# Optimization experiments

Hardware: AMD Instinct MI355X
Metric: run time of the kernel (lower is better)

## Reference

```python
import jax, jax.numpy as jnp
import numpy as np

B, T, F, U = 256, 512, 64, 128
MAX_TIMESTAMP = 100.0


def setup_inputs() -> dict:
    key = jax.random.key(0)
    ks = jax.random.split(key, 16)

    def w(k, shape, scale=0.05):
        return jax.random.normal(k, shape, dtype=jnp.float32) * scale

    return {
        "inputs": jax.random.uniform(ks[0], (B, T, 5 * F), dtype=jnp.float32),
        "h0": jnp.zeros((B, U), jnp.float32),
        "ts0": jnp.zeros((B, F), jnp.float32),
        "dt0": jnp.zeros((B, F), jnp.float32),
        "w_regression": w(ks[1], (U, F)),
        "b_regression": jnp.zeros((1,), jnp.float32),
        "w_controleur": w(ks[2], (U, F)),
        "b_controleur": jnp.zeros((F,), jnp.float32),
        "w_delta": w(ks[3], (F, U)),
        "b_delta": jnp.zeros((1,), jnp.float32),
        "w_value_mask": w(ks[4], (2 * F, U)),
        "b_value_mask": jnp.zeros((1,), jnp.float32),
        "w_corr": w(ks[5], (F, F)),
        "b_corr": jnp.zeros((F,), jnp.float32),
        "w_concat": w(ks[6], (F + U, F)),
        "b_concat": jnp.zeros((1,), jnp.float32),
        "u_update": w(ks[7], (U, U)),
        "w_update": w(ks[8], (2 * F, U)),
        "b_update": jnp.zeros((1,), jnp.float32),
        "u_reset": w(ks[9], (U, U)),
        "w_reset": w(ks[10], (2 * F, U)),
        "b_reset": jnp.zeros((1,), jnp.float32),
    }


def reference(inputs, h0, ts0, dt0,
              w_regression, b_regression, w_controleur, b_controleur,
              w_delta, b_delta, w_value_mask, b_value_mask,
              w_corr, b_corr, w_concat, b_concat,
              u_update, w_update, b_update,
              u_reset, w_reset, b_reset):
    nf = ts0.shape[1]
    off_diag = (1.0 - jnp.eye(nf, dtype=inputs.dtype))  # zero-diagonal mask on w_corr
    w_corr_masked = off_diag * w_corr

    def step(carry, x_t):
        h, prev_ts, prev_dt = carry
        ti = x_t[:, :nf]
        x_cur = x_t[:, nf:2 * nf]
        m = x_t[:, 2 * nf:3 * nf]
        dt = x_t[:, 3 * nf:4 * nf]
        pad = x_t[:, 4 * nf:5 * nf]

        x_reg = h @ w_regression + b_regression          # [B,F]
        # timestamp generation branch (is_timestamps_generated=True)
        tv = jnp.abs(h @ w_controleur + b_controleur)    # [B,F]
        ti = pad * ti + (1.0 - pad) * (prev_ts + tv)
        ti = jnp.where(ti <= MAX_TIMESTAMP, ti, prev_ts)
        d_gen = jnp.where(prev_ts + tv <= MAX_TIMESTAMP, tv, prev_dt)
        dt = pad * dt + (1.0 - pad) * d_gen

        x_cur = m * x_cur + (1.0 - m) * x_reg
        decay = jnp.exp(-jax.nn.relu(dt @ w_delta + b_delta))   # [B,U]
        z_corr = x_cur @ w_corr_masked + b_corr                  # [B,F]
        beta = jax.nn.sigmoid(jnp.concatenate([m, decay], 1) @ w_concat + b_concat)
        c_t = beta * z_corr + (1.0 - beta) * x_reg
        c = m * x_cur + (1.0 - m) * c_t

        cm = jnp.concatenate([c, m], 1)                  # [B,2F]
        dh = decay * h                                   # [B,U]
        z = jax.nn.sigmoid(dh @ u_update + cm @ w_update + b_update)
        r = jax.nn.sigmoid(dh @ u_reset + cm @ w_reset + b_reset)
        # NOTE: original code (faithfully) uses u_update in the candidate
        h_hat = jnp.tanh((r * dh) @ u_update + cm @ w_value_mask + b_value_mask)
        h_new = (1.0 - z) * h + z * h_hat

        out = jnp.concatenate([x_reg, z_corr, c, ti, dt], 1)  # [B,5F]
        return (h_new, ti, dt), out

    xs = jnp.swapaxes(inputs, 0, 1)  # [T,B,5F]
    (hT, tsT, dtT), out_seq = jax.lax.scan(step, (h0, ts0, dt0), xs)
    return out_seq, hT, tsT, dtT
```

## Files before the change

### kernel.cpp

```cpp
#include <hip/hip_runtime.h>
#include <stdint.h>


#define T_STEPS 512
#define BDIM 512

typedef unsigned int u32;
typedef u32 u32x4 __attribute__((ext_vector_type(4)));
typedef __fp16 f16;
typedef f16 h2 __attribute__((ext_vector_type(2)));

union pun { u32 u; h2 h; };
__device__ __forceinline__ u32 h2u(h2 h) { pun p; p.h = h; return p.u; }
__device__ __forceinline__ h2 u2h(u32 u) { pun p; p.u = u; return p.h; }
__device__ __forceinline__ h2 pkh(float a, float b) { return __builtin_amdgcn_cvt_pkrtz(a, b); }

__device__ __forceinline__ float dot2(h2 a, h2 b, float c) {
    return __builtin_amdgcn_fdot2(a, b, c, false);
}
__device__ __forceinline__ float sigm(float x) { return 1.0f / (1.0f + __expf(-x)); }
__device__ __forceinline__ float tanh_f(float x) { return 2.0f / (1.0f + __expf(-2.0f * x)) - 1.0f; }

__global__ __launch_bounds__(BDIM) __attribute__((amdgpu_waves_per_eu(2, 2)))
void padd_gru_kernel(
    const float* __restrict__ xin,
    const float* __restrict__ h0,
    const float* __restrict__ ts0,
    const float* __restrict__ dt0,
    const float* __restrict__ w_reg, const float* __restrict__ b_reg,
    const float* __restrict__ w_ctl, const float* __restrict__ b_ctl,
    const float* __restrict__ w_dlt, const float* __restrict__ b_dlt,
    const float* __restrict__ w_vm,  const float* __restrict__ b_vm,
    const float* __restrict__ w_cor, const float* __restrict__ b_cor,
    const float* __restrict__ w_cat, const float* __restrict__ b_cat,
    const float* __restrict__ u_upd, const float* __restrict__ w_upd, const float* __restrict__ b_upd,
    const float* __restrict__ u_rst, const float* __restrict__ w_rst, const float* __restrict__ b_rst,
    float* __restrict__ out)
{
    const int t = threadIdx.x;
    const int b = blockIdx.x;

    __shared__ float h32[128];
    __shared__ float outbuf[320];
    __shared__ float tv32[64];
    __shared__ float xcur32[64];
    __shared__ float m32[64];
    __shared__ float dh32[128];
    __shared__ float z32[128];
    __shared__ float xs[320];
    __shared__ float bctl32[64];
    __shared__ float bcor32[64];
    __shared__ __align__(16) u32 hpk[64];
    __shared__ __align__(16) u32 dtpk[32];
    __shared__ __align__(16) u32 xcpk[32];
    __shared__ __align__(16) u32 catpk[96];
    __shared__ __align__(16) u32 epk[128];
    __shared__ __align__(16) u32 rdhpk[64];

    const int s4 = t & 3, j4 = t >> 2;
    const int s8 = t & 7, j8 = t >> 3;
    const int s2 = t & 1, j2 = t >> 1;

    h2 wA[16];
    h2 wD[8];
    h2 wC[4];
    h2 wCt[12];
    h2 wE[64];
    h2 wF[32];

    {
        const float* src = (j4 < 64) ? (w_reg + j4) : (w_ctl + (j4 - 64));
        #pragma unroll
        for (int i = 0; i < 16; i++) {
            int k = 32 * s4 + 2 * i;
            wA[i] = pkh(src[k * 64], src[(k + 1) * 64]);
        }
    }
    {
        #pragma unroll
        for (int i = 0; i < 8; i++) {
            int k = 16 * s4 + 2 * i;
            wD[i] = pkh(w_dlt[k * 128 + j4], w_dlt[(k + 1) * 128 + j4]);
        }
    }
    {
        #pragma unroll
        for (int i = 0; i < 4; i++) {
            int k = 8 * s8 + 2 * i;
            float a = (k     == j8) ? 0.f : w_cor[k * 64 + j8];
            float c = (k + 1 == j8) ? 0.f : w_cor[(k + 1) * 64 + j8];
            wC[i] = pkh(a, c);
        }
    }
    {
        #pragma unroll
        for (int i = 0; i < 12; i++) {
            int k = 24 * s8 + 2 * i;
            wCt[i] = pkh(w_cat[k * 64 + j8], w_cat[(k + 1) * 64 + j8]);
        }
    }
    {
        const float* M = (j2 < 128) ? (s2 == 0 ? u_upd : w_upd)
                                    : (s2 == 0 ? u_rst : w_rst);
        const float* src = M + (j2 & 127);
        #pragma unroll
        for (int i = 0; i < 64; i++) {
            wE[i] = pkh(src[(2 * i) * 128], src[(2 * i + 1) * 128]);
        }
    }
    {
        const float* base = (s4 < 2) ? (u_upd + (64 * s4) * 128 + j4)
                                     : (w_vm + (64 * (s4 - 2)) * 128 + j4);
        #pragma unroll
        for (int i = 0; i < 32; i++) {
            wF[i] = pkh(base[(2 * i) * 128], base[(2 * i + 1) * 128]);
        }
    }

    const float bReg = b_reg[0];
    const float bDlt = b_dlt[0];
    const float bVm  = b_vm[0];
    const float bCat = b_cat[0];
    const float bUpd = b_upd[0];
    const float bRst = b_rst[0];

    if (t < 128) h32[t] = h0[(size_t)b * 128 + t];
    if (t < 64) {
        outbuf[192 + t] = ts0[(size_t)b * 64 + t];
        outbuf[256 + t] = dt0[(size_t)b * 64 + t];
        bctl32[t] = b_ctl[t];
        bcor32[t] = b_cor[t];
        hpk[t] = h2u(pkh(h0[(size_t)b * 128 + 2 * t], h0[(size_t)b * 128 + 2 * t + 1]));
    }

    float2 xpre;
    xpre.x = 0.f; xpre.y = 0.f;
    if (t < 160) {
        xpre = ((const float2*)(xin + (size_t)b * 512 * 320))[t];
    }

    __syncthreads();

    for (int st = 0; st < T_STEPS; ++st) {
        if (t < 160) {
            xs[2 * t]     = xpre.x;
            xs[2 * t + 1] = xpre.y;
            int stn = (st + 1 < T_STEPS) ? (st + 1) : st;
            xpre = ((const float2*)(xin + ((size_t)b * 512 + stn) * 320))[t];
        }

        {
            const u32x4* hp = (const u32x4*)&hpk[16 * s4];
            float a0 = 0.f, a1 = 0.f;
            #pragma unroll
            for (int q = 0; q < 4; q++) {
                u32x4 h4 = hp[q];
                a0 = dot2(wA[4*q+0], u2h(h4.x), a0);
                a1 = dot2(wA[4*q+1], u2h(h4.y), a1);
                a0 = dot2(wA[4*q+2], u2h(h4.z), a0);
                a1 = dot2(wA[4*q+3], u2h(h4.w), a1);
            }
            float v = a0 + a1;
            v += __shfl_xor(v, 1);
            v += __shfl_xor(v, 2);
            if (s4 == 0) {
                if (j4 < 64) outbuf[j4] = v + bReg;
                else         tv32[j4 - 64] = fabsf(v + bctl32[j4 - 64]);
            }
        }
        __syncthreads();

        if (t < 64) {
            float ti_in = xs[t], x_in = xs[64 + t], m = xs[128 + t];
            float dt_in = xs[192 + t], pad = xs[256 + t];
            float pts = outbuf[192 + t], pdt = outbuf[256 + t];
            float tv = tv32[t], xrg = outbuf[t];
            float sum = pts + tv;
            float tic = pad * ti_in + (1.f - pad) * sum;
            float tin = (tic <= 100.0f) ? tic : pts;
            float dg  = (sum <= 100.0f) ? tv : pdt;
            float dtn = pad * dt_in + (1.f - pad) * dg;
            float xc  = m * x_in + (1.f - m) * xrg;
            outbuf[192 + t] = tin;
            outbuf[256 + t] = dtn;
            xcur32[t] = xc;
            m32[t] = m;
            float dtn2 = __shfl_down(dtn, 1);
            float xc2  = __shfl_down(xc, 1);
            float m2   = __shfl_down(m, 1);
            if ((t & 1) == 0) {
                dtpk[t >> 1] = h2u(pkh(dtn, dtn2));
                xcpk[t >> 1] = h2u(pkh(xc, xc2));
                u32 mp = h2u(pkh(m, m2));
                catpk[t >> 1] = mp;
                epk[96 + (t >> 1)] = mp;
            }
        }
        __syncthreads();

        {
            const u32x4* dp = (const u32x4*)&dtpk[8 * s4];
            float a0 = 0.f, a1 = 0.f;
            #pragma unroll
            for (int q = 0; q < 2; q++) {
                u32x4 d4 = dp[q];
                a0 = dot2(wD[4*q+0], u2h(d4.x), a0);
                a1 = dot2(wD[4*q+1], u2h(d4.y), a1);
                a0 = dot2(wD[4*q+2], u2h(d4.z), a0);
                a1 = dot2(wD[4*q+3], u2h(d4.w), a1);
            }
            float vd = a0 + a1;
            vd += __shfl_xor(vd, 1);
            vd += __shfl_xor(vd, 2);

            u32x4 x4 = *(const u32x4*)&xcpk[4 * s8];
            float c0 = dot2(wC[0], u2h(x4.x), 0.f);
            float c1 = dot2(wC[1], u2h(x4.y), 0.f);
            c0 = dot2(wC[2], u2h(x4.z), c0);
            c1 = dot2(wC[3], u2h(x4.w), c1);
            float vc = c0 + c1;
            vc += __shfl_xor(vc, 1);
            vc += __shfl_xor(vc, 2);
            vc += __shfl_xor(vc, 4);

            float d  = __expf(-fmaxf(vd + bDlt, 0.f));
            float dh = d * h32[j4];
            float d2  = __shfl_down(d, 4);
            float dh2 = __shfl_down(dh, 4);
            if (s4 == 0) dh32[j4] = dh;
            if ((t & 7) == 0) {
                catpk[32 + (j4 >> 1)] = h2u(pkh(d, d2));
                epk[j4 >> 1]          = h2u(pkh(dh, dh2));
                outbuf[64 + j8] = vc + bcor32[j8];
            }
        }
        __syncthreads();

        {
            const u32x4* cp = (const u32x4*)&catpk[12 * s8];
            float a0 = 0.f, a1 = 0.f;
            #pragma unroll
            for (int q = 0; q < 3; q++) {
                u32x4 c4 = cp[q];
                a0 = dot2(wCt[4*q+0], u2h(c4.x), a0);
                a1 = dot2(wCt[4*q+1], u2h(c4.y), a1);
                a0 = dot2(wCt[4*q+2], u2h(c4.z), a0);
                a1 = dot2(wCt[4*q+3], u2h(c4.w), a1);
            }
            float v = a0 + a1;
            v += __shfl_xor(v, 1);
            v += __shfl_xor(v, 2);
            v += __shfl_xor(v, 4);
            float beta = sigm(v + bCat);
            float ct = beta * outbuf[64 + j8] + (1.f - beta) * outbuf[j8];
            float m  = m32[j8];
            float c  = m * xcur32[j8] + (1.f - m) * ct;
            float c2 = __shfl_down(c, 8);
            if (s8 == 0) outbuf[128 + j8] = c;
            if ((t & 15) == 0) epk[64 + (j8 >> 1)] = h2u(pkh(c, c2));
        }
        __syncthreads();

        {
            const u32x4* ep = (const u32x4*)&epk[64 * s2];
            float a0 = 0.f, a1 = 0.f, a2 = 0.f, a3 = 0.f;
            #pragma unroll
            for (int q = 0; q < 16; q++) {
                u32x4 e4 = ep[q];
                a0 = dot2(wE[4*q+0], u2h(e4.x), a0);
                a1 = dot2(wE[4*q+1], u2h(e4.y), a1);
                a2 = dot2(wE[4*q+2], u2h(e4.z), a2);
                a3 = dot2(wE[4*q+3], u2h(e4.w), a3);
            }
            float v = (a0 + a1) + (a2 + a3);
            v += __shfl_xor(v, 1);
            if (j2 < 128) {
                float z = sigm(v + bUpd);
                if (s2 == 0) z32[j2] = z;
            } else {
                float r = sigm(v + bRst);
                float rdh = r * dh32[j2 - 128];
                float rdh2 = __shfl_down(rdh, 2);
                if ((t & 3) == 0) rdhpk[(j2 - 128) >> 1] = h2u(pkh(rdh, rdh2));
            }
            if (t < 160) {
                float2 v2;
                v2.x = outbuf[2 * t];
                v2.y = outbuf[2 * t + 1];
                ((float2*)(out + ((size_t)st * 256 + b) * 320))[t] = v2;
            }
        }
        __syncthreads();

        {
            const u32x4* fp = (s4 & 2) ? (const u32x4*)&epk[64 + 32 * (s4 & 1)]
                                       : (const u32x4*)&rdhpk[32 * s4];
            float a0 = 0.f, a1 = 0.f;
            #pragma unroll
            for (int q = 0; q < 8; q++) {
                u32x4 f4 = fp[q];
                a0 = dot2(wF[4*q+0], u2h(f4.x), a0);
                a1 = dot2(wF[4*q+1], u2h(f4.y), a1);
                a0 = dot2(wF[4*q+2], u2h(f4.z), a0);
                a1 = dot2(wF[4*q+3], u2h(f4.w), a1);
            }
            float v = a0 + a1;
            v += __shfl_xor(v, 1);
            v += __shfl_xor(v, 2);
            float hh = tanh_f(v + bVm);
            float z = z32[j4];
            float hn = (1.f - z) * h32[j4] + z * hh;
            float hn2 = __shfl_down(hn, 4);
            if (s4 == 0) h32[j4] = hn;
            if ((t & 7) == 0) hpk[j4 >> 1] = h2u(pkh(hn, hn2));
        }
        __syncthreads();
    }

    if (t < 128) out[(size_t)41943040u + (size_t)b * 128 + t] = h32[t];
    if (t < 64) {
        out[(size_t)41975808u + (size_t)b * 64 + t] = outbuf[192 + t];
        out[(size_t)41992192u + (size_t)b * 64 + t] = outbuf[256 + t];
    }
}

extern "C" void kernel_launch(void* const* d_in, const int* in_sizes, int n_in,
                              void* d_out, int out_size, void* d_ws, size_t ws_size,
                              hipStream_t stream) {
    const float* xin   = (const float*)d_in[0];
    const float* h0    = (const float*)d_in[1];
    const float* ts0   = (const float*)d_in[2];
    const float* dt0   = (const float*)d_in[3];
    const float* w_reg = (const float*)d_in[4];
    const float* b_reg = (const float*)d_in[5];
    const float* w_ctl = (const float*)d_in[6];
    const float* b_ctl = (const float*)d_in[7];
    const float* w_dlt = (const float*)d_in[8];
    const float* b_dlt = (const float*)d_in[9];
    const float* w_vm  = (const float*)d_in[10];
    const float* b_vm  = (const float*)d_in[11];
    const float* w_cor = (const float*)d_in[12];
    const float* b_cor = (const float*)d_in[13];
    const float* w_cat = (const float*)d_in[14];
    const float* b_cat = (const float*)d_in[15];
    const float* u_upd = (const float*)d_in[16];
    const float* w_upd = (const float*)d_in[17];
    const float* b_upd = (const float*)d_in[18];
    const float* u_rst = (const float*)d_in[19];
    const float* w_rst = (const float*)d_in[20];
    const float* b_rst = (const float*)d_in[21];

    padd_gru_kernel<<<dim3(256), dim3(BDIM), 0, stream>>>(
        xin, h0, ts0, dt0,
        w_reg, b_reg, w_ctl, b_ctl, w_dlt, b_dlt, w_vm, b_vm,
        w_cor, b_cor, w_cat, b_cat,
        u_upd, w_upd, b_upd, u_rst, w_rst, b_rst,
        (float*)d_out);
}
```

Before: 1.496 ms.

## Remap lanes for DPP/permlane reductions and fold elementwise stage into matvec

Result: faster. 1.340 ms (-10.4%).

```diff
diff --git a/kernel.cpp b/kernel.cpp
--- a/kernel.cpp
+++ b/kernel.cpp
@@ -21,7 +21,43 @@
 __device__ __forceinline__ float sigm(float x) { return 1.0f / (1.0f + __expf(-x)); }
 __device__ __forceinline__ float tanh_f(float x) { return 2.0f / (1.0f + __expf(-2.0f * x)) - 1.0f; }
 
-__global__ __launch_bounds__(BDIM) __attribute__((amdgpu_waves_per_eu(2, 2)))
+template<int CTRL>
+__device__ __forceinline__ float qadd(float v) {
+    int p = __builtin_amdgcn_update_dpp(0, __float_as_int(v), CTRL, 0xF, 0xF, true);
+    return v + __int_as_float(p);
+}
+template<int CTRL>
+__device__ __forceinline__ float qxchg(float v) {
+    return __int_as_float(__builtin_amdgcn_update_dpp(0, __float_as_int(v), CTRL, 0xF, 0xF, true));
+}
+__device__ __forceinline__ float x16sum(float v) {
+#if __has_builtin(__builtin_amdgcn_permlane16_swap)
+    auto r = __builtin_amdgcn_permlane16_swap(__float_as_uint(v), __float_as_uint(v), false, false);
+    return __uint_as_float(r[0]) + __uint_as_float(r[1]);
+#else
+    return v + __shfl_xor(v, 16);
+#endif
+}
+__device__ __forceinline__ float x16get(float v, int l) {
+#if __has_builtin(__builtin_amdgcn_permlane16_swap)
+    auto r = __builtin_amdgcn_permlane16_swap(__float_as_uint(v), __float_as_uint(v), false, false);
+    return __uint_as_float((l & 16) ? r[0] : r[1]);
+#else
+    return __shfl_xor(v, 16);
+#endif
+}
+__device__ __forceinline__ float x32get(float v, int l) {
+#if __has_builtin(__builtin_amdgcn_permlane32_swap)
+    auto r = __builtin_amdgcn_permlane32_swap(__float_as_uint(v), __float_as_uint(v), false, false);
+    return __uint_as_float((l & 32) ? r[0] : r[1]);
+#else
+    return __shfl_xor(v, 32);
+#endif
+}
+
+__device__ __forceinline__ int klo(int p) { return (p & 3) + 8 * (p >> 2); }
+
+__global__ __launch_bounds__(BDIM, 2)
 void padd_gru_kernel(
     const float* __restrict__ xin,
     const float* __restrict__ h0,
@@ -42,7 +78,6 @@
 
     __shared__ float h32[128];
     __shared__ float outbuf[320];
-    __shared__ float tv32[64];
     __shared__ float xcur32[64];
     __shared__ float m32[64];
     __shared__ float dh32[128];
@@ -57,9 +92,15 @@
     __shared__ __align__(16) u32 epk[128];
     __shared__ __align__(16) u32 rdhpk[64];
 
-    const int s4 = t & 3, j4 = t >> 2;
-    const int s8 = t & 7, j8 = t >> 3;
-    const int s2 = t & 1, j2 = t >> 1;
+    const int l = t & 63, w = t >> 6;
+    const int sA = l & 3;
+    const int b23 = (l >> 2) & 3;
+    const int b4 = (l >> 4) & 1, b5 = (l >> 5) & 1;
+    const int fA = b23 + 4 * b5 + 8 * w;
+    const int uCF = b23 + 4 * ((l >> 4) & 3) + 16 * w;
+    const int s8 = (l & 3) | (b4 << 2);
+    const int s2 = l & 1;
+    const int jE = ((l >> 1) & 31) + 32 * w;
 
     h2 wA[16];
     h2 wD[8];
@@ -69,51 +110,61 @@
     h2 wF[32];
 
     {
-        const float* src = (j4 < 64) ? (w_reg + j4) : (w_ctl + (j4 - 64));
+        const float* src = b4 ? (w_ctl + fA) : (w_reg + fA);
         #pragma unroll
         for (int i = 0; i < 16; i++) {
-            int k = 32 * s4 + 2 * i;
-            wA[i] = pkh(src[k * 64], src[(k + 1) * 64]);
+            int k = klo(16 * sA + i);
+            wA[i] = pkh(src[k * 64], src[(k + 4) * 64]);
         }
     }
     {
         #pragma unroll
         for (int i = 0; i < 8; i++) {
-            int k = 16 * s4 + 2 * i;
-            wD[i] = pkh(w_dlt[k * 128 + j4], w_dlt[(k + 1) * 128 + j4]);
+            int k = klo(8 * sA + i);
+            wD[i] = pkh(w_dlt[k * 128 + uCF], w_dlt[(k + 4) * 128 + uCF]);
         }
     }
     {
         #pragma unroll
         for (int i = 0; i < 4; i++) {
-            int k = 8 * s8 + 2 * i;
-            float a = (k     == j8) ? 0.f : w_cor[k * 64 + j8];
-            float c = (k + 1 == j8) ? 0.f : w_cor[(k + 1) * 64 + j8];
+            int k = klo(4 * s8 + i);
+            float a = (k     == fA) ? 0.f : w_cor[k * 64 + fA];
+            float c = (k + 4 == fA) ? 0.f : w_cor[(k + 4) * 64 + fA];
             wC[i] = pkh(a, c);
         }
     }
     {
         #pragma unroll
         for (int i = 0; i < 12; i++) {
-            int k = 24 * s8 + 2 * i;
-            wCt[i] = pkh(w_cat[k * 64 + j8], w_cat[(k + 1) * 64 + j8]);
-        }
-    }
-    {
-        const float* M = (j2 < 128) ? (s2 == 0 ? u_upd : w_upd)
-                                    : (s2 == 0 ? u_rst : w_rst);
-        const float* src = M + (j2 & 127);
+            int sig = 12 * s8 + i;
+            int r0 = (sig < 32) ? klo(sig) : 64 + klo(sig - 32);
+            wCt[i] = pkh(w_cat[r0 * 64 + fA], w_cat[(r0 + 4) * 64 + fA]);
+        }
+    }
+    {
+        const float* MU = (jE < 128) ? u_upd : u_rst;
+        const float* MW = (jE < 128) ? w_upd : w_rst;
+        const int cj = jE & 127;
         #pragma unroll
         for (int i = 0; i < 64; i++) {
-            wE[i] = pkh(src[(2 * i) * 128], src[(2 * i + 1) * 128]);
-        }
-    }
-    {
-        const float* base = (s4 < 2) ? (u_upd + (64 * s4) * 128 + j4)
-                                     : (w_vm + (64 * (s4 - 2)) * 128 + j4);
+            int sig = 64 * s2 + i;
+            const float* M; int r0;
+            if (sig < 64)      { M = MU; r0 = klo(sig); }
+            else if (sig < 96) { M = MW; r0 = klo(sig - 64); }
+            else               { M = MW; r0 = 64 + klo(sig - 96); }
+            wE[i] = pkh(M[r0 * 128 + cj], M[(r0 + 4) * 128 + cj]);
+        }
+    }
+    {
         #pragma unroll
         for (int i = 0; i < 32; i++) {
-            wF[i] = pkh(base[(2 * i) * 128], base[(2 * i + 1) * 128]);
+            int sig = 32 * sA + i;
+            if (sig < 64) {
+                wF[i] = pkh(u_upd[(2 * sig) * 128 + uCF], u_upd[(2 * sig + 1) * 128 + uCF]);
+            } else {
+                int k = (sig < 96) ? klo(sig - 64) : 64 + klo(sig - 96);
+                wF[i] = pkh(w_vm[k * 128 + uCF], w_vm[(k + 4) * 128 + uCF]);
+            }
         }
     }
 
@@ -130,27 +181,21 @@
         outbuf[256 + t] = dt0[(size_t)b * 64 + t];
         bctl32[t] = b_ctl[t];
         bcor32[t] = b_cor[t];
-        hpk[t] = h2u(pkh(h0[(size_t)b * 128 + 2 * t], h0[(size_t)b * 128 + 2 * t + 1]));
-    }
-
-    float2 xpre;
-    xpre.x = 0.f; xpre.y = 0.f;
+        int u = klo(t);
+        hpk[t] = h2u(pkh(h0[(size_t)b * 128 + u], h0[(size_t)b * 128 + u + 4]));
+    }
+
+    float2 xpre; xpre.x = 0.f; xpre.y = 0.f;
     if (t < 160) {
-        xpre = ((const float2*)(xin + (size_t)b * 512 * 320))[t];
-    }
-
+        float2 x0 = ((const float2*)(xin + (size_t)b * 512 * 320))[t];
+        xs[2 * t] = x0.x; xs[2 * t + 1] = x0.y;
+        xpre = ((const float2*)(xin + ((size_t)b * 512 + 1) * 320))[t];
+    }
     __syncthreads();
 
     for (int st = 0; st < T_STEPS; ++st) {
-        if (t < 160) {
-            xs[2 * t]     = xpre.x;
-            xs[2 * t + 1] = xpre.y;
-            int stn = (st + 1 < T_STEPS) ? (st + 1) : st;
-            xpre = ((const float2*)(xin + ((size_t)b * 512 + stn) * 320))[t];
-        }
-
-        {
-            const u32x4* hp = (const u32x4*)&hpk[16 * s4];
+        {
+            const u32x4* hp = (const u32x4*)&hpk[16 * sA];
             float a0 = 0.f, a1 = 0.f;
             #pragma unroll
             for (int q = 0; q < 4; q++) {
@@ -160,46 +205,39 @@
                 a0 = dot2(wA[4*q+2], u2h(h4.z), a0);
                 a1 = dot2(wA[4*q+3], u2h(h4.w), a1);
             }
-            float v = a0 + a1;
-            v += __shfl_xor(v, 1);
-            v += __shfl_xor(v, 2);
-            if (s4 == 0) {
-                if (j4 < 64) outbuf[j4] = v + bReg;
-                else         tv32[j4 - 64] = fabsf(v + bctl32[j4 - 64]);
-            }
-        }
-        __syncthreads();
-
-        if (t < 64) {
-            float ti_in = xs[t], x_in = xs[64 + t], m = xs[128 + t];
-            float dt_in = xs[192 + t], pad = xs[256 + t];
-            float pts = outbuf[192 + t], pdt = outbuf[256 + t];
-            float tv = tv32[t], xrg = outbuf[t];
+            float pre = qadd<0x4E>(qadd<0xB1>(a0 + a1));
+            float oth = x16get(pre, l);
+            float xrg = ((l & 16) ? oth : pre) + bReg;
+            float tv  = fabsf(((l & 16) ? pre : oth) + bctl32[fA]);
+            float ti_in = xs[fA], x_in = xs[64 + fA], m = xs[128 + fA];
+            float dt_in = xs[192 + fA], pad = xs[256 + fA];
+            float pts = outbuf[192 + fA], pdt = outbuf[256 + fA];
             float sum = pts + tv;
             float tic = pad * ti_in + (1.f - pad) * sum;
             float tin = (tic <= 100.0f) ? tic : pts;
             float dg  = (sum <= 100.0f) ? tv : pdt;
             float dtn = pad * dt_in + (1.f - pad) * dg;
             float xc  = m * x_in + (1.f - m) * xrg;
-            outbuf[192 + t] = tin;
-            outbuf[256 + t] = dtn;
-            xcur32[t] = xc;
-            m32[t] = m;
-            float dtn2 = __shfl_down(dtn, 1);
-            float xc2  = __shfl_down(xc, 1);
-            float m2   = __shfl_down(m, 1);
-            if ((t & 1) == 0) {
-                dtpk[t >> 1] = h2u(pkh(dtn, dtn2));
-                xcpk[t >> 1] = h2u(pkh(xc, xc2));
+            float dtn2 = x32get(dtn, l);
+            float xc2  = x32get(xc, l);
+            float m2   = x32get(m, l);
+            if ((l & 19) == 0) {
+                outbuf[192 + fA] = tin;
+                outbuf[256 + fA] = dtn;
+                xcur32[fA] = xc; m32[fA] = m; outbuf[fA] = xrg;
+            }
+            if ((l & 51) == 0) {
+                int p = b23 | (w << 2);
+                dtpk[p] = h2u(pkh(dtn, dtn2));
+                xcpk[p] = h2u(pkh(xc, xc2));
                 u32 mp = h2u(pkh(m, m2));
-                catpk[t >> 1] = mp;
-                epk[96 + (t >> 1)] = mp;
-            }
-        }
-        __syncthreads();
-
-        {
-            const u32x4* dp = (const u32x4*)&dtpk[8 * s4];
+                catpk[p] = mp; epk[96 + p] = mp;
+            }
+        }
+        __syncthreads();
+
+        {
+            const u32x4* dp = (const u32x4*)&dtpk[8 * sA];
             float a0 = 0.f, a1 = 0.f;
             #pragma unroll
             for (int q = 0; q < 2; q++) {
@@ -209,29 +247,25 @@
                 a0 = dot2(wD[4*q+2], u2h(d4.z), a0);
                 a1 = dot2(wD[4*q+3], u2h(d4.w), a1);
             }
-            float vd = a0 + a1;
-            vd += __shfl_xor(vd, 1);
-            vd += __shfl_xor(vd, 2);
+            float vd = qadd<0x4E>(qadd<0xB1>(a0 + a1));
 
             u32x4 x4 = *(const u32x4*)&xcpk[4 * s8];
             float c0 = dot2(wC[0], u2h(x4.x), 0.f);
             float c1 = dot2(wC[1], u2h(x4.y), 0.f);
             c0 = dot2(wC[2], u2h(x4.z), c0);
             c1 = dot2(wC[3], u2h(x4.w), c1);
-            float vc = c0 + c1;
-            vc += __shfl_xor(vc, 1);
-            vc += __shfl_xor(vc, 2);
-            vc += __shfl_xor(vc, 4);
+            float vc = x16sum(qadd<0x4E>(qadd<0xB1>(c0 + c1)));
 
             float d  = __expf(-fmaxf(vd + bDlt, 0.f));
-            float dh = d * h32[j4];
-            float d2  = __shfl_down(d, 4);
-            float dh2 = __shfl_down(dh, 4);
-            if (s4 == 0) dh32[j4] = dh;
-            if ((t & 7) == 0) {
-                catpk[32 + (j4 >> 1)] = h2u(pkh(d, d2));
-                epk[j4 >> 1]          = h2u(pkh(dh, dh2));
-                outbuf[64 + j8] = vc + bcor32[j8];
+            float dh = d * h32[uCF];
+            float d2  = x16get(d, l);
+            float dh2 = x16get(dh, l);
+            if ((l & 3) == 0) dh32[uCF] = dh;
+            if ((l & 19) == 0) {
+                int q = b23 | ((b5 | (w << 1)) << 2);
+                catpk[32 + q] = h2u(pkh(d, d2));
+                epk[q]        = h2u(pkh(dh, dh2));
+                outbuf[64 + fA] = vc + bcor32[fA];
             }
         }
         __syncthreads();
@@ -247,17 +281,14 @@
                 a0 = dot2(wCt[4*q+2], u2h(c4.z), a0);
                 a1 = dot2(wCt[4*q+3], u2h(c4.w), a1);
             }
-            float v = a0 + a1;
-            v += __shfl_xor(v, 1);
-            v += __shfl_xor(v, 2);
-            v += __shfl_xor(v, 4);
+            float v = x16sum(qadd<0x4E>(qadd<0xB1>(a0 + a1)));
             float beta = sigm(v + bCat);
-            float ct = beta * outbuf[64 + j8] + (1.f - beta) * outbuf[j8];
-            float m  = m32[j8];
-            float c  = m * xcur32[j8] + (1.f - m) * ct;
-            float c2 = __shfl_down(c, 8);
-            if (s8 == 0) outbuf[128 + j8] = c;
-            if ((t & 15) == 0) epk[64 + (j8 >> 1)] = h2u(pkh(c, c2));
+            float ct = beta * outbuf[64 + fA] + (1.f - beta) * outbuf[fA];
+            float m  = m32[fA];
+            float c  = m * xcur32[fA] + (1.f - m) * ct;
+            float c2 = x32get(c, l);
+            if ((l & 19) == 0) outbuf[128 + fA] = c;
+            if ((l & 51) == 0) epk[64 + (b23 | (w << 2))] = h2u(pkh(c, c2));
         }
         __syncthreads();
 
@@ -272,29 +303,30 @@
                 a2 = dot2(wE[4*q+2], u2h(e4.z), a2);
                 a3 = dot2(wE[4*q+3], u2h(e4.w), a3);
             }
-            float v = (a0 + a1) + (a2 + a3);
-            v += __shfl_xor(v, 1);
-            if (j2 < 128) {
+            float v = qadd<0xB1>((a0 + a1) + (a2 + a3));
+            if (jE < 128) {
                 float z = sigm(v + bUpd);
-                if (s2 == 0) z32[j2] = z;
+                if ((l & 1) == 0) z32[jE] = z;
             } else {
                 float r = sigm(v + bRst);
-                float rdh = r * dh32[j2 - 128];
-                float rdh2 = __shfl_down(rdh, 2);
-                if ((t & 3) == 0) rdhpk[(j2 - 128) >> 1] = h2u(pkh(rdh, rdh2));
+                float rdh = r * dh32[jE - 128];
+                float rdh2 = qxchg<0x4E>(rdh);
+                if ((l & 3) == 0) rdhpk[(jE - 128) >> 1] = h2u(pkh(rdh, rdh2));
             }
             if (t < 160) {
                 float2 v2;
-                v2.x = outbuf[2 * t];
-                v2.y = outbuf[2 * t + 1];
+                v2.x = outbuf[2 * t]; v2.y = outbuf[2 * t + 1];
                 ((float2*)(out + ((size_t)st * 256 + b) * 320))[t] = v2;
-            }
-        }
-        __syncthreads();
-
-        {
-            const u32x4* fp = (s4 & 2) ? (const u32x4*)&epk[64 + 32 * (s4 & 1)]
-                                       : (const u32x4*)&rdhpk[32 * s4];
+                xs[2 * t] = xpre.x; xs[2 * t + 1] = xpre.y;
+                int stn = (st + 2 < T_STEPS) ? (st + 2) : (T_STEPS - 1);
+                xpre = ((const float2*)(xin + ((size_t)b * 512 + stn) * 320))[t];
+            }
+        }
+        __syncthreads();
+
+        {
+            const u32x4* fp = (sA < 2) ? (const u32x4*)&rdhpk[32 * sA]
+                                       : (const u32x4*)&epk[64 + 32 * (sA - 2)];
             float a0 = 0.f, a1 = 0.f;
             #pragma unroll
             for (int q = 0; q < 8; q++) {
@@ -304,15 +336,13 @@
                 a0 = dot2(wF[4*q+2], u2h(f4.z), a0);
                 a1 = dot2(wF[4*q+3], u2h(f4.w), a1);
             }
-            float v = a0 + a1;
-            v += __shfl_xor(v, 1);
-            v += __shfl_xor(v, 2);
+            float v = qadd<0x4E>(qadd<0xB1>(a0 + a1));
             float hh = tanh_f(v + bVm);
-            float z = z32[j4];
-            float hn = (1.f - z) * h32[j4] + z * hh;
-            float hn2 = __shfl_down(hn, 4);
-            if (s4 == 0) h32[j4] = hn;
-            if ((t & 7) == 0) hpk[j4 >> 1] = h2u(pkh(hn, hn2));
+            float z = z32[uCF];
+            float hn = (1.f - z) * h32[uCF] + z * hh;
+            float hn2 = x16get(hn, l);
+            if ((l & 3) == 0) h32[uCF] = hn;
+            if ((l & 19) == 0) hpk[b23 | ((b5 | (w << 1)) << 2)] = h2u(pkh(hn, hn2));
         }
         __syncthreads();
     }
```
